# Performance work log

Hardware: AMD Instinct MI355X
Metric: run time of the kernel (lower is better)

The kernel has to match this reference:

```python
import jax, jax.numpy as jnp
import numpy as np

NUM_HEADS = 8
NUM_LEVELS = 4
NUM_POINTS = 4
EMBED = 256
HEAD_DIM = EMBED // NUM_HEADS
SPATIAL = [(100, 100), (50, 50), (25, 25), (13, 13)]  # (H, W) per level


def _bilinear_sample(val, grid):
    """torch.nn.functional.grid_sample(mode='bilinear', padding_mode='zeros', align_corners=False).
    val: [B, H, W, C], grid: [B, N, 2] with (x, y) in [-1, 1]. Returns [B, N, C]."""
    B, H, W, C = val.shape
    x = (grid[..., 0] + 1.0) * (W * 0.5) - 0.5
    y = (grid[..., 1] + 1.0) * (H * 0.5) - 0.5
    x0 = jnp.floor(x)
    y0 = jnp.floor(y)
    wx1 = x - x0
    wy1 = y - y0
    wx0 = 1.0 - wx1
    wy0 = 1.0 - wy1
    x0i = x0.astype(jnp.int32)
    y0i = y0.astype(jnp.int32)
    valf = val.reshape(B, H * W, C)

    def corner(xi, yi, w):
        valid = (xi >= 0) & (xi < W) & (yi >= 0) & (yi < H)
        idx = jnp.clip(yi, 0, H - 1) * W + jnp.clip(xi, 0, W - 1)
        v = jnp.take_along_axis(valf, idx[..., None], axis=1)  # [B, N, C]
        return v * (w * valid)[..., None]

    return (corner(x0i, y0i, wx0 * wy0) + corner(x0i + 1, y0i, wx1 * wy0)
            + corner(x0i, y0i + 1, wx0 * wy1) + corner(x0i + 1, y0i + 1, wx1 * wy1))


def setup_inputs() -> dict:
    key = jax.random.key(0)
    ks = jax.random.split(key, 12)
    bs, nq = 4, 6000
    nv = sum(h * w for h, w in SPATIAL)
    s = 0.02
    return {
        "query": jax.random.normal(ks[0], (bs, nq, EMBED), jnp.float32),
        "value": jax.random.normal(ks[1], (bs, nv, EMBED), jnp.float32),
        "reference_points": jax.random.uniform(ks[2], (bs, nq, NUM_LEVELS, 2), jnp.float32),
        "W_off": jax.random.normal(ks[3], (EMBED, NUM_HEADS * NUM_LEVELS * NUM_POINTS * 2), jnp.float32) * s,
        "b_off": jax.random.normal(ks[4], (NUM_HEADS * NUM_LEVELS * NUM_POINTS * 2,), jnp.float32),
        "W_attn": jax.random.normal(ks[5], (EMBED, NUM_HEADS * NUM_LEVELS * NUM_POINTS), jnp.float32) * s,
        "b_attn": jnp.zeros((NUM_HEADS * NUM_LEVELS * NUM_POINTS,), jnp.float32),
        "W_val": jax.random.normal(ks[6], (EMBED, EMBED), jnp.float32) * s,
        "b_val": jnp.zeros((EMBED,), jnp.float32),
        "W_out": jax.random.normal(ks[7], (EMBED, EMBED), jnp.float32) * s,
        "b_out": jnp.zeros((EMBED,), jnp.float32),
        "spatial_shapes": jnp.asarray(np.array(SPATIAL, dtype=np.int32)),
    }


def reference(query, value, reference_points, W_off, b_off, W_attn, b_attn,
              W_val, b_val, W_out, b_out, spatial_shapes):
    shapes = [(int(h), int(w)) for h, w in np.asarray(spatial_shapes)]
    bs, nq, _ = query.shape
    nv = value.shape[1]

    v = (value @ W_val + b_val).reshape(bs, nv, NUM_HEADS, HEAD_DIM)
    offsets = (query @ W_off + b_off).reshape(bs, nq, NUM_HEADS, NUM_LEVELS, NUM_POINTS, 2)
    aw = (query @ W_attn + b_attn).reshape(bs, nq, NUM_HEADS, NUM_LEVELS * NUM_POINTS)
    aw = jax.nn.softmax(aw, axis=-1).reshape(bs, nq, NUM_HEADS, NUM_LEVELS, NUM_POINTS)

    # offset normalizer is [W, H] per level
    norm = jnp.asarray([[w, h] for h, w in shapes], dtype=query.dtype)  # [L, 2]
    loc = reference_points[:, :, None, :, None, :] + offsets / norm[None, None, None, :, None, :]
    grids = 2.0 * loc - 1.0  # [bs, nq, H, L, P, 2]
    # -> [bs*H, nq*P, 2] per level
    grids = jnp.transpose(grids, (0, 2, 1, 3, 4, 5)).reshape(bs * NUM_HEADS, nq, NUM_LEVELS, NUM_POINTS, 2)

    v_bh = jnp.transpose(v, (0, 2, 1, 3)).reshape(bs * NUM_HEADS, nv, HEAD_DIM)
    sampled = []
    start = 0
    for l, (H_, W_) in enumerate(shapes):
        val_l = v_bh[:, start:start + H_ * W_].reshape(bs * NUM_HEADS, H_, W_, HEAD_DIM)
        grid_l = grids[:, :, l].reshape(bs * NUM_HEADS, nq * NUM_POINTS, 2)
        s_l = _bilinear_sample(val_l, grid_l).reshape(bs * NUM_HEADS, nq, NUM_POINTS, HEAD_DIM)
        sampled.append(s_l)
        start += H_ * W_
    sampled = jnp.stack(sampled, axis=2)  # [bs*H, nq, L, P, c]

    aw_bh = jnp.transpose(aw, (0, 2, 1, 3, 4)).reshape(bs * NUM_HEADS, nq, NUM_LEVELS, NUM_POINTS)
    out = (sampled * aw_bh[..., None]).sum(axis=(2, 3))  # [bs*H, nq, c]
    out = out.reshape(bs, NUM_HEADS, nq, HEAD_DIM).transpose(0, 2, 1, 3).reshape(bs, nq, EMBED)
    out = out @ W_out + b_out
    return out + query
```

## Files before the change

kernel.cpp:

```cpp
#include <hip/hip_runtime.h>
#include <hip/hip_bf16.h>

#define BS 4
#define NQ 6000
#define NV 13294
#define NH 8
#define HD 32
#define EMB 256
#define MV (BS * NV)
#define MQ (BS * NQ)

typedef __attribute__((ext_vector_type(8))) short short8;
typedef __attribute__((ext_vector_type(4))) float floatx4;

__device__ __constant__ float LVL_DIM[4] = {100.f, 50.f, 25.f, 13.f};

__device__ inline unsigned short bf16bits(float f) {
  __hip_bfloat16 h = __float2bfloat16(f);
  return *reinterpret_cast<unsigned short*>(&h);
}
__device__ inline unsigned int pk2bf(float lo, float hi) {
  return (unsigned int)bf16bits(lo) | ((unsigned int)bf16bits(hi) << 16);
}
__device__ inline float bflo(unsigned int u) { return __uint_as_float(u << 16); }
__device__ inline float bfhi(unsigned int u) { return __uint_as_float(u & 0xffff0000u); }

#define LDSTR 40
#define TILEU (128 * LDSTR)

__global__ __launch_bounds__(256) void wtrans_kernel(
    const float* __restrict__ W_val, const float* __restrict__ W_off,
    const float* __restrict__ W_attn, const float* __restrict__ W_out,
    unsigned short* __restrict__ Wt_val, unsigned short* __restrict__ Wt_qcat,
    unsigned short* __restrict__ Wt_out) {
  const int b = blockIdx.x, k = threadIdx.x;
  if (b < 256) {
    Wt_val[b * EMB + k] = bf16bits(W_val[k * 256 + b]);
  } else if (b < 640) {
    const int n = b - 256;
    float v = (n < 256) ? W_off[k * 256 + n] : W_attn[k * 128 + (n - 256)];
    Wt_qcat[n * EMB + k] = bf16bits(v);
  } else {
    const int n = b - 640;
    Wt_out[n * EMB + k] = bf16bits(W_out[k * 256 + n]);
  }
}

__device__ inline void loadA32(const float* __restrict__ A, int M, int m0,
                               int k0, int tid, float4 ra[4]) {
  const int r = tid >> 1, kh = (tid & 1) * 16;
  const int row = m0 + r;
  if (row < M) {
    const float* src = A + (size_t)row * EMB + k0 + kh;
#pragma unroll
    for (int j = 0; j < 4; ++j) ra[j] = *(const float4*)(src + 4 * j);
  } else {
#pragma unroll
    for (int j = 0; j < 4; ++j) ra[j] = make_float4(0.f, 0.f, 0.f, 0.f);
  }
}
__device__ inline void storeA32(unsigned short* lds, int tid,
                                const float4 ra[4]) {
  const int r = tid >> 1, kh = (tid & 1) * 16;
  unsigned short* dst = lds + r * LDSTR + kh;
  uint4 u0, u1;
  u0.x = pk2bf(ra[0].x, ra[0].y);
  u0.y = pk2bf(ra[0].z, ra[0].w);
  u0.z = pk2bf(ra[1].x, ra[1].y);
  u0.w = pk2bf(ra[1].z, ra[1].w);
  u1.x = pk2bf(ra[2].x, ra[2].y);
  u1.y = pk2bf(ra[2].z, ra[2].w);
  u1.z = pk2bf(ra[3].x, ra[3].y);
  u1.w = pk2bf(ra[3].z, ra[3].w);
  *(uint4*)(dst) = u0;
  *(uint4*)(dst + 8) = u1;
}
__device__ inline void loadBb(const unsigned short* __restrict__ B, int NB,
                              int n0, int k0, int tid, uint4 rb[2]) {
  const int r = tid >> 1, kh = (tid & 1) * 16;
  const int row = n0 + r;
  if (row < NB) {
    const unsigned short* src = B + (size_t)row * EMB + k0 + kh;
    rb[0] = *(const uint4*)(src);
    rb[1] = *(const uint4*)(src + 8);
  } else {
    rb[0] = make_uint4(0, 0, 0, 0);
    rb[1] = make_uint4(0, 0, 0, 0);
  }
}
__device__ inline void storeBb(unsigned short* lds, int tid,
                               const uint4 rb[2]) {
  const int r = tid >> 1, kh = (tid & 1) * 16;
  unsigned short* dst = lds + r * LDSTR + kh;
  *(uint4*)(dst) = rb[0];
  *(uint4*)(dst + 8) = rb[1];
}

__device__ inline void mfma_step32(const unsigned short* ldsA,
                                   const unsigned short* ldsB, int wm, int wn,
                                   int lane, floatx4 acc[4][4]) {
  const unsigned short* ap =
      ldsA + (wm * 64 + (lane & 15)) * LDSTR + (lane >> 4) * 8;
  const unsigned short* bp =
      ldsB + (wn * 64 + (lane & 15)) * LDSTR + (lane >> 4) * 8;
  short8 af[4], bfr[4];
#pragma unroll
  for (int t = 0; t < 4; ++t) {
    af[t] = *(const short8*)(ap + t * 16 * LDSTR);
    bfr[t] = *(const short8*)(bp + t * 16 * LDSTR);
  }
#pragma unroll
  for (int mt = 0; mt < 4; ++mt)
#pragma unroll
    for (int nt = 0; nt < 4; ++nt)
      acc[mt][nt] = __builtin_amdgcn_mfma_f32_16x16x32_bf16(af[mt], bfr[nt],
                                                            acc[mt][nt], 0, 0, 0);
}

__device__ inline void gemm_loop32_f32A(const float* __restrict__ A, int M,
                                        int m0,
                                        const unsigned short* __restrict__ B,
                                        int NB, int n0, unsigned short* lds,
                                        int tid, int wm, int wn, int lane,
                                        floatx4 acc[4][4]) {
  unsigned short* bufA[2] = {lds, lds + 2 * TILEU};
  unsigned short* bufB[2] = {lds + TILEU, lds + 3 * TILEU};
  float4 sa[2][4];
  uint4 sb[2][2];
  loadA32(A, M, m0, 0, tid, sa[0]);
  loadBb(B, NB, n0, 0, tid, sb[0]);
  loadA32(A, M, m0, 32, tid, sa[1]);
  loadBb(B, NB, n0, 32, tid, sb[1]);
  storeA32(bufA[0], tid, sa[0]);
  storeBb(bufB[0], tid, sb[0]);
  __syncthreads();
#pragma unroll
  for (int k = 0; k < 8; ++k) {
    const int cur = k & 1, nxt = cur ^ 1;
    if (k + 2 < 8) {
      loadA32(A, M, m0, (k + 2) * 32, tid, sa[k & 1]);
      loadBb(B, NB, n0, (k + 2) * 32, tid, sb[k & 1]);
    }
    if (k + 1 < 8) {
      storeA32(bufA[nxt], tid, sa[(k + 1) & 1]);
      storeBb(bufB[nxt], tid, sb[(k + 1) & 1]);
    }
    mfma_step32(bufA[cur], bufB[cur], wm, wn, lane, acc);
    __syncthreads();
  }
}

__device__ inline void gemm_loop32_bf16A(const unsigned short* __restrict__ A,
                                         int M, int m0,
                                         const unsigned short* __restrict__ B,
                                         int NB, int n0, unsigned short* lds,
                                         int tid, int wm, int wn, int lane,
                                         floatx4 acc[4][4]) {
  unsigned short* bufA[2] = {lds, lds + 2 * TILEU};
  unsigned short* bufB[2] = {lds + TILEU, lds + 3 * TILEU};
  uint4 sa[2][2], sb[2][2];
  loadBb(A, M, m0, 0, tid, sa[0]);
  loadBb(B, NB, n0, 0, tid, sb[0]);
  loadBb(A, M, m0, 32, tid, sa[1]);
  loadBb(B, NB, n0, 32, tid, sb[1]);
  storeBb(bufA[0], tid, sa[0]);
  storeBb(bufB[0], tid, sb[0]);
  __syncthreads();
#pragma unroll
  for (int k = 0; k < 8; ++k) {
    const int cur = k & 1, nxt = cur ^ 1;
    if (k + 2 < 8) {
      loadBb(A, M, m0, (k + 2) * 32, tid, sa[k & 1]);
      loadBb(B, NB, n0, (k + 2) * 32, tid, sb[k & 1]);
    }
    if (k + 1 < 8) {
      storeBb(bufA[nxt], tid, sa[(k + 1) & 1]);
      storeBb(bufB[nxt], tid, sb[(k + 1) & 1]);
    }
    mfma_step32(bufA[cur], bufB[cur], wm, wn, lane, acc);
    __syncthreads();
  }
}

__global__ __launch_bounds__(256, 2) void vqproj_kernel(
    const float* __restrict__ value, const unsigned short* __restrict__ Wt_val,
    const float* __restrict__ b_val, unsigned short* __restrict__ vbh,
    const float* __restrict__ query, const unsigned short* __restrict__ Wt_qcat,
    const float* __restrict__ refpts, const float* __restrict__ b_off,
    const float* __restrict__ b_attn, float* __restrict__ locbuf,
    float* __restrict__ awbuf) {
  __shared__ unsigned short lds[4 * TILEU];
  const int tid = threadIdx.x, lane = tid & 63, w = tid >> 6;
  const int wm = w >> 1, wn = w & 1;
  floatx4 acc[4][4];
  const floatx4 zero = {0.f, 0.f, 0.f, 0.f};
#pragma unroll
  for (int i2 = 0; i2 < 4; i2++)
#pragma unroll
    for (int j = 0; j < 4; j++) acc[i2][j] = zero;
  const int quad = lane >> 4, cl = lane & 15;

  if (blockIdx.x < 832) {
    const int chunk = blockIdx.x >> 4, i = blockIdx.x & 15;
    const int m0 = (chunk * 8 + (i & 7)) * 128;
    const int n0 = (i >> 3) * 128;
    gemm_loop32_f32A(value, MV, m0, Wt_val, 256, n0, lds, tid, wm, wn, lane,
                     acc);
#pragma unroll
    for (int mt = 0; mt < 4; ++mt) {
#pragma unroll
      for (int r = 0; r < 4; ++r) {
        const int row = m0 + wm * 64 + mt * 16 + quad * 4 + r;
        if (row < MV) {
          const int b = row / NV, n = row - b * NV;
#pragma unroll
          for (int nt = 0; nt < 4; ++nt) {
            const int c = n0 + wn * 64 + nt * 16 + cl;
            const int h = c >> 5, d = c & 31;
            vbh[(((size_t)(b * NH + h)) * NV + n) * HD + d] =
                bf16bits(acc[mt][nt][r] + b_val[c]);
          }
        }
      }
    }
  } else {
    const int bid = blockIdx.x - 832;
    const int chunk = bid / 24, i = bid % 24;
    const int m_idx = chunk * 8 + (i & 7);
    if (m_idx >= 188) return;
    const int m0 = m_idx * 128;
    const int n0 = (i >> 3) * 128;
    gemm_loop32_f32A(query, MQ, m0, Wt_qcat, 384, n0, lds, tid, wm, wn, lane,
                     acc);
    if (n0 < 256) {
#pragma unroll
      for (int mt = 0; mt < 4; ++mt) {
#pragma unroll
        for (int r = 0; r < 4; ++r) {
          const int row = m0 + wm * 64 + mt * 16 + quad * 4 + r;
          if (row < MQ) {
#pragma unroll
            for (int nt = 0; nt < 4; ++nt) {
              const int c = n0 + wn * 64 + nt * 16 + cl;
              const int xy = c & 1, l = (c >> 3) & 3;
              const float dim = LVL_DIM[l];
              const float ref = refpts[(size_t)row * 8 + l * 2 + xy];
              locbuf[(size_t)row * 256 + c] =
                  ref * dim + acc[mt][nt][r] + b_off[c] - 0.5f;
            }
          }
        }
      }
    } else {
#pragma unroll
      for (int mt = 0; mt < 4; ++mt) {
#pragma unroll
        for (int r = 0; r < 4; ++r) {
          const int row = m0 + wm * 64 + mt * 16 + quad * 4 + r;
          if (row < MQ) {
#pragma unroll
            for (int nt = 0; nt < 4; ++nt) {
              const int ca = wn * 64 + nt * 16 + cl;
              awbuf[(size_t)row * 128 + ca] = acc[mt][nt][r] + b_attn[ca];
            }
          }
        }
      }
    }
  }
}

__global__ __launch_bounds__(256, 4) void sample_kernel(
    const unsigned short* __restrict__ vbh, const float* __restrict__ locbuf,
    const float* __restrict__ awbuf, unsigned short* __restrict__ sampledb) {
  const int blk = blockIdx.x;
  const int t = blk >> 3;
  const int quarter = t / 750;
  const int j = t - quarter * 750;
  const int slice = (blk & 7) * 4 + quarter;
  const int h = slice & 7;
  const int w = threadIdx.x >> 6;
  const int lane = threadIdx.x & 63;
  const int r0 = (slice >> 3) * NQ + j * 8 + w * 2;
  const int g = lane >> 2;
  const int d8 = lane & 3;
  const int l = g >> 2;

  const int W_ = (l < 2) ? ((l == 0) ? 100 : 50) : ((l == 2) ? 25 : 13);
  const int START = (l < 2) ? ((l == 0) ? 0 : 10000) : ((l == 2) ? 12500 : 13125);
  const unsigned int* base =
      (const unsigned int*)vbh + ((size_t)slice * NV + START) * 16 + d8 * 4;

  float acc0[8], acc1[8];
#pragma unroll
  for (int rr = 0; rr < 2; ++rr) {
    const int row = r0 + rr;
    float* a = rr ? acc1 : acc0;
    const float2 xy =
        *(const float2*)(locbuf + (size_t)row * 256 + h * 32 + g * 2);
    const float wl = awbuf[(size_t)row * 128 + h * 16 + g];
    float mx = wl;
    mx = fmaxf(mx, __shfl_xor(mx, 4));
    mx = fmaxf(mx, __shfl_xor(mx, 8));
    mx = fmaxf(mx, __shfl_xor(mx, 16));
    mx = fmaxf(mx, __shfl_xor(mx, 32));
    const float e = __expf(wl - mx);
    float ssum = e;
    ssum += __shfl_xor(ssum, 4);
    ssum += __shfl_xor(ssum, 8);
    ssum += __shfl_xor(ssum, 16);
    ssum += __shfl_xor(ssum, 32);
    const float wgt = e / ssum;

    const float fx = floorf(xy.x), fy = floorf(xy.y);
    const int x0 = (int)fx, y0 = (int)fy;
    const float wx1 = xy.x - fx, wy1 = xy.y - fy;
    const float wx0 = 1.f - wx1, wy0 = 1.f - wy1;
    const int x0c = min(max(x0, 0), W_ - 1), x1c = min(max(x0 + 1, 0), W_ - 1);
    const int y0c = min(max(y0, 0), W_ - 1), y1c = min(max(y0 + 1, 0), W_ - 1);
    const float mx0 = ((unsigned)x0 < (unsigned)W_) ? wx0 : 0.f;
    const float mx1 = ((unsigned)(x0 + 1) < (unsigned)W_) ? wx1 : 0.f;
    const float my0 = ((unsigned)y0 < (unsigned)W_) ? wy0 : 0.f;
    const float my1 = ((unsigned)(y0 + 1) < (unsigned)W_) ? wy1 : 0.f;
    const float wy0w = wgt * my0, wy1w = wgt * my1;
    const float w00 = wy0w * mx0, w01 = wy0w * mx1;
    const float w10 = wy1w * mx0, w11 = wy1w * mx1;

    const int rb0 = y0c * W_, rb1 = y1c * W_;
    const uint4 u00 = *(const uint4*)(base + (size_t)(rb0 + x0c) * 16);
    const uint4 u01 = *(const uint4*)(base + (size_t)(rb0 + x1c) * 16);
    const uint4 u10 = *(const uint4*)(base + (size_t)(rb1 + x0c) * 16);
    const uint4 u11 = *(const uint4*)(base + (size_t)(rb1 + x1c) * 16);
    const unsigned int* p00 = &u00.x;
    const unsigned int* p01 = &u01.x;
    const unsigned int* p10 = &u10.x;
    const unsigned int* p11 = &u11.x;
#pragma unroll
    for (int k = 0; k < 4; ++k) {
      a[2 * k] = w00 * bflo(p00[k]) + w01 * bflo(p01[k]) + w10 * bflo(p10[k]) +
                 w11 * bflo(p11[k]);
      a[2 * k + 1] = w00 * bfhi(p00[k]) + w01 * bfhi(p01[k]) +
                     w10 * bfhi(p10[k]) + w11 * bfhi(p11[k]);
    }
  }

  const bool b0 = (lane >> 2) & 1;
  const bool b1 = (lane >> 3) & 1;
  const bool b2 = (lane >> 4) & 1;
#pragma unroll
  for (int rr = 0; rr < 2; ++rr) {
    float* v = rr ? acc1 : acc0;
#pragma unroll
    for (int jj = 0; jj < 4; ++jj) {
      float lo = v[jj], hi = v[jj + 4];
      float recv = __shfl_xor(b0 ? lo : hi, 4);
      v[jj] = (b0 ? hi : lo) + recv;
    }
#pragma unroll
    for (int jj = 0; jj < 2; ++jj) {
      float lo = v[jj], hi = v[jj + 2];
      float recv = __shfl_xor(b1 ? lo : hi, 8);
      v[jj] = (b1 ? hi : lo) + recv;
    }
    {
      float lo = v[0], hi = v[1];
      float recv = __shfl_xor(b2 ? lo : hi, 16);
      v[0] = (b2 ? hi : lo) + recv;
    }
    v[0] += __shfl_xor(v[0], 32);
  }

  const int dim = d8 * 8 + (b0 ? 4 : 0) + (b1 ? 2 : 0) + (b2 ? 1 : 0);
  const int row = (lane < 32) ? r0 : (r0 + 1);
  const float val = (lane < 32) ? acc0[0] : acc1[0];
  sampledb[(size_t)row * EMB + h * 32 + dim] = bf16bits(val);
}

__global__ __launch_bounds__(256, 2) void oproj_kernel(
    const unsigned short* __restrict__ sampledb,
    const unsigned short* __restrict__ Wt, const float* __restrict__ b_out,
    const float* __restrict__ query, float* __restrict__ out) {
  __shared__ unsigned short lds[4 * TILEU];
  const int tid = threadIdx.x, lane = tid & 63, w = tid >> 6;
  const int wm = w >> 1, wn = w & 1;
  const int chunk = blockIdx.x >> 4, i = blockIdx.x & 15;
  const int m_idx = chunk * 8 + (i & 7);
  if (m_idx >= 188) return;
  const int m0 = m_idx * 128;
  const int n0 = (i >> 3) * 128;
  floatx4 acc[4][4];
  const floatx4 zero = {0.f, 0.f, 0.f, 0.f};
#pragma unroll
  for (int i2 = 0; i2 < 4; i2++)
#pragma unroll
    for (int j = 0; j < 4; j++) acc[i2][j] = zero;

  gemm_loop32_bf16A(sampledb, MQ, m0, Wt, 256, n0, lds, tid, wm, wn, lane,
                    acc);

  const int quad = lane >> 4, cl = lane & 15;
#pragma unroll
  for (int mt = 0; mt < 4; ++mt) {
#pragma unroll
    for (int r = 0; r < 4; ++r) {
      const int row = m0 + wm * 64 + mt * 16 + quad * 4 + r;
      if (row < MQ) {
#pragma unroll
        for (int nt = 0; nt < 4; ++nt) {
          const int c = n0 + wn * 64 + nt * 16 + cl;
          out[(size_t)row * EMB + c] =
              acc[mt][nt][r] + b_out[c] + query[(size_t)row * EMB + c];
        }
      }
    }
  }
}

extern "C" void kernel_launch(void* const* d_in, const int* in_sizes, int n_in,
                              void* d_out, int out_size, void* d_ws,
                              size_t ws_size, hipStream_t stream) {
  const float* query  = (const float*)d_in[0];
  const float* value  = (const float*)d_in[1];
  const float* refpts = (const float*)d_in[2];
  const float* W_off  = (const float*)d_in[3];
  const float* b_off  = (const float*)d_in[4];
  const float* W_attn = (const float*)d_in[5];
  const float* b_attn = (const float*)d_in[6];
  const float* W_val  = (const float*)d_in[7];
  const float* b_val  = (const float*)d_in[8];
  const float* W_out  = (const float*)d_in[9];
  const float* b_out  = (const float*)d_in[10];
  float* out = (float*)d_out;

  char* ws = (char*)d_ws;
  unsigned short* vbh = (unsigned short*)ws;
  float* locbuf = (float*)(ws + 27226112);
  float* awbuf = (float*)(ws + 51802112);
  unsigned short* sampledb = (unsigned short*)(ws + 64090112);
  unsigned short* Wt_val = (unsigned short*)(ws + 76378112);
  unsigned short* Wt_qcat = (unsigned short*)(ws + 76509184);
  unsigned short* Wt_out = (unsigned short*)(ws + 76705792);

  wtrans_kernel<<<896, 256, 0, stream>>>(W_val, W_off, W_attn, W_out, Wt_val,
                                         Wt_qcat, Wt_out);
  vqproj_kernel<<<1408, 256, 0, stream>>>(value, Wt_val, b_val, vbh, query,
                                          Wt_qcat, refpts, b_off, b_attn,
                                          locbuf, awbuf);
  sample_kernel<<<24000, 256, 0, stream>>>(vbh, locbuf, awbuf, sampledb);
  oproj_kernel<<<384, 256, 0, stream>>>(sampledb, Wt_out, b_out, query, out);
}
```

Baseline: 239.7 us.

## Tile weight transpose via LDS, sample four rows per wave, shrink LDS stride

The weight transpose kernel now uses 32x32 shared-memory tiles, so both its reads and writes are coalesced, and it runs on far fewer blocks. The sampling kernel now has each wave process four query rows instead of two, which halves the grid and gives each thread more independent gathers to overlap, at the cost of more registers. The LDS row stride for the GEMM tiles changes from 40 to 36, which may alter bank-conflict behaviour and alignment of the vector LDS accesses.

Measured after the change: 280.0 us. 1.17x slower.

```diff
diff --git a/kernel.cpp b/kernel.cpp
--- a/kernel.cpp
+++ b/kernel.cpp
@@ -25,7 +25,7 @@
 __device__ inline float bflo(unsigned int u) { return __uint_as_float(u << 16); }
 __device__ inline float bfhi(unsigned int u) { return __uint_as_float(u & 0xffff0000u); }
 
-#define LDSTR 40
+#define LDSTR 36
 #define TILEU (128 * LDSTR)
 
 __global__ __launch_bounds__(256) void wtrans_kernel(
@@ -33,17 +33,53 @@
     const float* __restrict__ W_attn, const float* __restrict__ W_out,
     unsigned short* __restrict__ Wt_val, unsigned short* __restrict__ Wt_qcat,
     unsigned short* __restrict__ Wt_out) {
-  const int b = blockIdx.x, k = threadIdx.x;
-  if (b < 256) {
-    Wt_val[b * EMB + k] = bf16bits(W_val[k * 256 + b]);
-  } else if (b < 640) {
-    const int n = b - 256;
-    float v = (n < 256) ? W_off[k * 256 + n] : W_attn[k * 128 + (n - 256)];
-    Wt_qcat[n * EMB + k] = bf16bits(v);
+  __shared__ float tile[32][33];
+  const int b = blockIdx.x;
+  const int x = threadIdx.x & 31, ty = threadIdx.x >> 5;
+
+  const float* src;
+  unsigned short* dst;
+  int k0, n0;
+  if (b < 64) {
+    src = W_val;
+    dst = Wt_val;
+    k0 = (b >> 3) * 32;
+    n0 = (b & 7) * 32;
+  } else if (b < 128) {
+    const int bb = b - 64;
+    src = W_off;
+    dst = Wt_qcat;
+    k0 = (bb >> 3) * 32;
+    n0 = (bb & 7) * 32;
+  } else if (b < 160) {
+    const int bb = b - 128;
+    src = W_attn;
+    dst = Wt_qcat + 256 * EMB;
+    k0 = (bb >> 2) * 32;
+    n0 = (bb & 3) * 32;
+#pragma unroll
+    for (int i = 0; i < 4; ++i)
+      tile[ty + 8 * i][x] = src[(size_t)(k0 + ty + 8 * i) * 128 + n0 + x];
+    __syncthreads();
+#pragma unroll
+    for (int i = 0; i < 4; ++i)
+      dst[(size_t)(n0 + ty + 8 * i) * EMB + k0 + x] =
+          bf16bits(tile[x][ty + 8 * i]);
+    return;
   } else {
-    const int n = b - 640;
-    Wt_out[n * EMB + k] = bf16bits(W_out[k * 256 + n]);
-  }
+    const int bb = b - 160;
+    src = W_out;
+    dst = Wt_out;
+    k0 = (bb >> 3) * 32;
+    n0 = (bb & 7) * 32;
+  }
+#pragma unroll
+  for (int i = 0; i < 4; ++i)
+    tile[ty + 8 * i][x] = src[(size_t)(k0 + ty + 8 * i) * 256 + n0 + x];
+  __syncthreads();
+#pragma unroll
+  for (int i = 0; i < 4; ++i)
+    dst[(size_t)(n0 + ty + 8 * i) * EMB + k0 + x] = bf16bits(tile[x][ty + 8 * i]);
 }
 
 __device__ inline void loadA32(const float* __restrict__ A, int M, int m0,
@@ -275,13 +311,13 @@
     const float* __restrict__ awbuf, unsigned short* __restrict__ sampledb) {
   const int blk = blockIdx.x;
   const int t = blk >> 3;
-  const int quarter = t / 750;
-  const int j = t - quarter * 750;
+  const int quarter = t / 375;
+  const int j = t - quarter * 375;
   const int slice = (blk & 7) * 4 + quarter;
   const int h = slice & 7;
   const int w = threadIdx.x >> 6;
   const int lane = threadIdx.x & 63;
-  const int r0 = (slice >> 3) * NQ + j * 8 + w * 2;
+  const int r0 = (slice >> 3) * NQ + j * 16 + w * 4;
   const int g = lane >> 2;
   const int d8 = lane & 3;
   const int l = g >> 2;
@@ -291,11 +327,10 @@
   const unsigned int* base =
       (const unsigned int*)vbh + ((size_t)slice * NV + START) * 16 + d8 * 4;
 
-  float acc0[8], acc1[8];
-#pragma unroll
-  for (int rr = 0; rr < 2; ++rr) {
+  float acc[4][8];
+#pragma unroll
+  for (int rr = 0; rr < 4; ++rr) {
     const int row = r0 + rr;
-    float* a = rr ? acc1 : acc0;
     const float2 xy =
         *(const float2*)(locbuf + (size_t)row * 256 + h * 32 + g * 2);
     const float wl = awbuf[(size_t)row * 128 + h * 16 + g];
@@ -337,10 +372,10 @@
     const unsigned int* p11 = &u11.x;
 #pragma unroll
     for (int k = 0; k < 4; ++k) {
-      a[2 * k] = w00 * bflo(p00[k]) + w01 * bflo(p01[k]) + w10 * bflo(p10[k]) +
-                 w11 * bflo(p11[k]);
-      a[2 * k + 1] = w00 * bfhi(p00[k]) + w01 * bfhi(p01[k]) +
-                     w10 * bfhi(p10[k]) + w11 * bfhi(p11[k]);
+      acc[rr][2 * k] = w00 * bflo(p00[k]) + w01 * bflo(p01[k]) +
+                       w10 * bflo(p10[k]) + w11 * bflo(p11[k]);
+      acc[rr][2 * k + 1] = w00 * bfhi(p00[k]) + w01 * bfhi(p01[k]) +
+                           w10 * bfhi(p10[k]) + w11 * bfhi(p11[k]);
     }
   }
 
@@ -348,8 +383,8 @@
   const bool b1 = (lane >> 3) & 1;
   const bool b2 = (lane >> 4) & 1;
 #pragma unroll
-  for (int rr = 0; rr < 2; ++rr) {
-    float* v = rr ? acc1 : acc0;
+  for (int rr = 0; rr < 4; ++rr) {
+    float* v = acc[rr];
 #pragma unroll
     for (int jj = 0; jj < 4; ++jj) {
       float lo = v[jj], hi = v[jj + 4];
@@ -371,9 +406,13 @@
   }
 
   const int dim = d8 * 8 + (b0 ? 4 : 0) + (b1 ? 2 : 0) + (b2 ? 1 : 0);
-  const int row = (lane < 32) ? r0 : (r0 + 1);
-  const float val = (lane < 32) ? acc0[0] : acc1[0];
-  sampledb[(size_t)row * EMB + h * 32 + dim] = bf16bits(val);
+  const bool hi = (lane >= 32);
+  const float v0 = hi ? acc[1][0] : acc[0][0];
+  const float v1 = hi ? acc[3][0] : acc[2][0];
+  const int row0 = r0 + (hi ? 1 : 0);
+  const int row1 = r0 + 2 + (hi ? 1 : 0);
+  sampledb[(size_t)row0 * EMB + h * 32 + dim] = bf16bits(v0);
+  sampledb[(size_t)row1 * EMB + h * 32 + dim] = bf16bits(v1);
 }
 
 __global__ __launch_bounds__(256, 2) void oproj_kernel(
@@ -441,11 +480,11 @@
   unsigned short* Wt_qcat = (unsigned short*)(ws + 76509184);
   unsigned short* Wt_out = (unsigned short*)(ws + 76705792);
 
-  wtrans_kernel<<<896, 256, 0, stream>>>(W_val, W_off, W_attn, W_out, Wt_val,
+  wtrans_kernel<<<224, 256, 0, stream>>>(W_val, W_off, W_attn, W_out, Wt_val,
                                          Wt_qcat, Wt_out);
   vqproj_kernel<<<1408, 256, 0, stream>>>(value, Wt_val, b_val, vbh, query,
                                           Wt_qcat, refpts, b_off, b_attn,
                                           locbuf, awbuf);
-  sample_kernel<<<24000, 256, 0, stream>>>(vbh, locbuf, awbuf, sampledb);
+  sample_kernel<<<12000, 256, 0, stream>>>(vbh, locbuf, awbuf, sampledb);
   oproj_kernel<<<384, 256, 0, stream>>>(sampledb, Wt_out, b_out, query, out);
 }
```
